# Kernel optimization log

Hardware: AMD Instinct MI355X
Metric: run time of the kernel (lower is better)

Reference implementation:

```python
import jax, jax.numpy as jnp
import numpy as np

N, n, m, k = 100000, 32, 16, 32
MU = 100.0  # bubble kernel scale (init arg mu)


def setup_inputs() -> dict:
    key = jax.random.key(0)
    ks = jax.random.split(key, 7)
    x = jax.random.normal(ks[0], (N,), dtype=jnp.float32)
    # torch.nn.Linear(N, n): weight [n, N], bias [n]
    encoder_w = jax.random.normal(ks[1], (n, N), dtype=jnp.float32) / np.float32(np.sqrt(N))
    encoder_b = jnp.zeros((n,), dtype=jnp.float32)
    # decoder parameter [n, N]
    decoder = jax.random.normal(ks[2], (n, N), dtype=jnp.float32) / np.float32(np.sqrt(n))
    # torch.nn.Linear(n, n*m): weight [n*m, n], bias [n*m]
    bw_w = jax.random.normal(ks[3], (n * m, n), dtype=jnp.float32) / np.float32(np.sqrt(n))
    bw_b = jnp.zeros((n * m,), dtype=jnp.float32)
    neighbour_distance = jax.random.uniform(ks[4], (N, k), dtype=jnp.float32)
    neighbour_id = jax.random.randint(ks[5], (N, k), 0, N)
    clustering_labels = jax.random.randint(ks[6], (N,), 0, m)
    return {
        "x": x,
        "encoder_w": encoder_w,
        "encoder_b": encoder_b,
        "decoder": decoder,
        "bw_w": bw_w,
        "bw_b": bw_b,
        "neighbour_distance": neighbour_distance,
        "neighbour_id": neighbour_id,
        "clustering_labels": clustering_labels,
    }


def reference(x, encoder_w, encoder_b, decoder, bw_w, bw_b,
              neighbour_distance, neighbour_id, clustering_labels):
    # encode: [N] -> [n]
    encoded = x @ encoder_w.T + encoder_b
    # per-basis, per-cluster bandwidths: sigmoid(Linear)/60 -> [n, m] -> expand to [n, N]
    bandwidths = jax.nn.sigmoid(encoded @ bw_w.T + bw_b) / 60.0
    w = bandwidths.reshape(n, m)[:, clustering_labels]  # [n, N]
    # bubble window: relu(1 - d^2 / (w*mu)^2) -> [n, N, k]
    window = jax.nn.relu(1.0 - neighbour_distance[None, :, :] ** 2
                         / (w[:, :, None] * MU) ** 2)
    # normalization over axis 1 (the N axis), faithful to the source's dim=1
    window = window / jnp.sum(window, axis=1, keepdims=True)
    # gather decoder rows at neighbours, weight, reduce over k: [n, N]
    convolved_basis = jnp.sum(decoder[:, neighbour_id] * window, axis=-1)
    # [n] @ [n, N] -> [N]
    return encoded @ convolved_basis
```

## Files before the change

### kernel.cpp

```cpp
#include <hip/hip_runtime.h>
#include <hip/hip_fp16.h>

#define N_PTS 100000
#define MU_F  100.0f
#define BUCKET 8192

typedef unsigned int uint;
typedef _Float16 h2 __attribute__((ext_vector_type(2)));
typedef float f2 __attribute__((ext_vector_type(2)));

#define E_SCALE 16384.0f
#define E_SCALE_INV (1.0f / 16384.0f)

static __device__ inline h2 h2pack(float a, float b) {
    return __builtin_bit_cast(h2, __builtin_amdgcn_cvt_pkrtz(a, b));
}
static __device__ inline float fdot2f(h2 a, h2 b, float c) {
    return __builtin_amdgcn_fdot2(a, b, c, false);
}
static __device__ inline h2 h2fma(h2 a, h2 b, h2 c) {
#if __has_builtin(__builtin_elementwise_fma)
    return __builtin_elementwise_fma(a, b, c);
#else
    return a * b + c;
#endif
}
static __device__ inline h2 h2max(h2 a, h2 b) {
#if __has_builtin(__builtin_elementwise_max)
    return __builtin_elementwise_max(a, b);
#else
    h2 r;
    r.x = a.x > b.x ? a.x : b.x;
    r.y = a.y > b.y ? a.y : b.y;
    return r;
#endif
}

#define ENC_BLKS 800
#define TR_BLKS  1563
#define SC_BLKS  196

__global__ __launch_bounds__(256) void k_prep(const float* __restrict__ x,
                                              const float* __restrict__ encW,
                                              const float* __restrict__ encB,
                                              const float* __restrict__ dec,
                                              const int* __restrict__ labels,
                                              float* __restrict__ enc,
                                              __half* __restrict__ decT,
                                              int* __restrict__ gcur,
                                              int* __restrict__ perm) {
    int b = blockIdx.x;
    if (b < ENC_BLKS) {
        int row = b & 31;
        int chunk = b >> 5;
        const int CH = 4000;
        int base = chunk * CH;
        const float4* W4 = reinterpret_cast<const float4*>(encW + (size_t)row * N_PTS + base);
        const float4* x4 = reinterpret_cast<const float4*>(x + base);
        const int nv = CH / 4;
        float acc = 0.f;
        for (int idx = threadIdx.x; idx < nv; idx += 256) {
            float4 w = W4[idx];
            float4 xv = x4[idx];
            acc += w.x * xv.x + w.y * xv.y + w.z * xv.z + w.w * xv.w;
        }
        #pragma unroll
        for (int off = 32; off > 0; off >>= 1) acc += __shfl_down(acc, off);
        __shared__ float sred[4];
        int wid = threadIdx.x >> 6;
        if ((threadIdx.x & 63) == 0) sred[wid] = acc;
        __syncthreads();
        if (threadIdx.x == 0) {
            float s = sred[0] + sred[1] + sred[2] + sred[3];
            if (chunk == 0) s += encB[row];
            atomicAdd(enc + row, s);
        }
    } else if (b < ENC_BLKS + TR_BLKS) {
        __shared__ float tile[32][65];
        int j0 = (b - ENC_BLKS) * 64;
        int col = threadIdx.x & 63;
        int r0 = threadIdx.x >> 6;
        #pragma unroll
        for (int it = 0; it < 8; ++it) {
            int row = it * 4 + r0;
            int j = j0 + col;
            float v = (j < N_PTS) ? dec[(size_t)row * N_PTS + j] : 0.f;
            tile[row][col] = v;
        }
        __syncthreads();
        #pragma unroll
        for (int it = 0; it < 4; ++it) {
            int idx = it * 256 + threadIdx.x;
            int j = idx >> 4;
            int p = idx & 15;
            int jj = j0 + j;
            if (jj < N_PTS) {
                __half2 h = __halves2half2(__float2half(tile[2 * p][j]),
                                           __float2half(tile[2 * p + 1][j]));
                *reinterpret_cast<__half2*>(decT + (size_t)jj * 32 + 2 * p) = h;
            }
        }
    } else {
        __shared__ int lh[16], lbase[16], lcur[16];
        const int CHUNK = 512;
        int start = (b - ENC_BLKS - TR_BLKS) * CHUNK;
        int end = min(start + CHUNK, N_PTS);
        if (threadIdx.x < 16) { lh[threadIdx.x] = 0; lcur[threadIdx.x] = 0; }
        __syncthreads();
        for (int j = start + threadIdx.x; j < end; j += 256)
            atomicAdd(&lh[labels[j]], 1);
        __syncthreads();
        if (threadIdx.x < 16)
            lbase[threadIdx.x] = threadIdx.x * BUCKET +
                                 atomicAdd(&gcur[threadIdx.x], lh[threadIdx.x]);
        __syncthreads();
        for (int j = start + threadIdx.x; j < end; j += 256) {
            int c = labels[j];
            int lpos = atomicAdd(&lcur[c], 1);
            perm[lbase[c] + lpos] = j;
        }
    }
}

__device__ inline void build_invC(const float* __restrict__ encL,
                                  const float* __restrict__ bw_w,
                                  const float* __restrict__ bw_b,
                                  float* __restrict__ invCL, int c) {
    if (threadIdx.x < 32) {
        int r = threadIdx.x * 16 + c;
        float z = bw_b[r];
        const float* wr = bw_w + r * 32;
        #pragma unroll
        for (int p = 0; p < 32; ++p) z = fmaf(encL[p], wr[p], z);
        float s = 1.f / (1.f + __expf(-z));
        float wmu = s * (MU_F / 60.0f);
        invCL[threadIdx.x] = 1.f / (wmu * wmu);
    }
}

__global__ __launch_bounds__(256, 4) void k_S_sorted(const float* __restrict__ enc_g,
                                                     const float* __restrict__ bw_w,
                                                     const float* __restrict__ bw_b,
                                                     const float* __restrict__ nd,
                                                     const int* __restrict__ perm,
                                                     const int* __restrict__ gcur,
                                                     float* __restrict__ S) {
    __shared__ float encL[32], invCL[32];
    __shared__ float Sloc[1024];
    int b = blockIdx.x;
    int c = b & 15;
    int ch = b >> 4;
    if (threadIdx.x < 32) encL[threadIdx.x] = enc_g[threadIdx.x];
    for (int t = threadIdx.x; t < 1024; t += 256) Sloc[t] = 0.f;
    __syncthreads();
    build_invC(encL, bw_w, bw_b, invCL, c);
    __syncthreads();

    f2 inv2[16];
    #pragma unroll
    for (int t = 0; t < 16; ++t) { inv2[t].x = invCL[2 * t]; inv2[t].y = invCL[2 * t + 1]; }

    int bs = c * BUCKET;
    int cnt = gcur[c];
    int lane = threadIdx.x & 63;
    int kk = lane & 31;
    int jh = lane >> 5;
    int gw = ch * 4 + (threadIdx.x >> 6);
    const int nw = 64 * 4;
    int npairs = (cnt + 1) >> 1;

    f2 acc2[16];
    #pragma unroll
    for (int t = 0; t < 16; ++t) { acc2[t].x = 0.f; acc2[t].y = 0.f; }

    if (gw < npairs) {
        auto ld = [&](int pc, float& d, bool& v) {
            bool ok = pc < npairs;
            v = ok && (2 * pc + jh) < cnt;
            int p = v ? (bs + 2 * pc + jh) : bs;
            int j = __builtin_nontemporal_load(&perm[p]);
            d = __builtin_nontemporal_load(&nd[(size_t)j * 32 + kk]);
        };
        int pp = gw;
        float dA, dB; bool vA, vB;
        ld(pp, dA, vA);
        ld(pp + nw, dB, vB);
        while (pp < npairs) {
            float dC; bool vC;
            ld(pp + 2 * nw, dC, vC);
            float d2 = vA ? dA * dA : 1e30f;
            f2 md2; md2.x = -d2; md2.y = -d2;
            f2 onev; onev.x = 1.f; onev.y = 1.f;
            #pragma unroll
            for (int t = 0; t < 16; ++t) {
                f2 w = md2 * inv2[t] + onev;
                w.x = fmaxf(w.x, 0.f);
                w.y = fmaxf(w.y, 0.f);
                acc2[t] += w;
            }
            dA = dB; vA = vB; dB = dC; vB = vC;
            pp += nw;
        }
    }
    #pragma unroll
    for (int t = 0; t < 16; ++t) {
        acc2[t].x += __shfl_xor(acc2[t].x, 32);
        acc2[t].y += __shfl_xor(acc2[t].y, 32);
    }
    if (jh == 0) {
        #pragma unroll
        for (int t = 0; t < 16; ++t) {
            atomicAdd(&Sloc[(2 * t) * 32 + kk], acc2[t].x);
            atomicAdd(&Sloc[(2 * t + 1) * 32 + kk], acc2[t].y);
        }
    }
    __syncthreads();
    for (int t = threadIdx.x; t < 1024; t += 256) {
        float v = Sloc[t];
        if (v != 0.f) atomicAdd(&S[t], v);
    }
}

__global__ __launch_bounds__(256, 8) void k_main(const float* __restrict__ enc_g,
                                                 const float* __restrict__ bw_w,
                                                 const float* __restrict__ bw_b,
                                                 const float* __restrict__ S_g,
                                                 const float* __restrict__ nd,
                                                 const int* __restrict__ nid,
                                                 const int* __restrict__ perm,
                                                 const int* __restrict__ gcur,
                                                 const __half* __restrict__ decT,
                                                 float* __restrict__ out) {
    __shared__ float encL[32], invCL[32];
    __shared__ float ELf[1024];
    int c = blockIdx.x & 15;
    int ch = blockIdx.x >> 4;
    if (threadIdx.x < 32) encL[threadIdx.x] = enc_g[threadIdx.x];
    __syncthreads();
    build_invC(encL, bw_w, bw_b, invCL, c);
    for (int t = threadIdx.x; t < 1024; t += 256)
        ELf[t] = encL[t >> 5] / S_g[t] * E_SCALE;
    __syncthreads();

    int lane = threadIdx.x & 63;
    int R = lane >> 2;
    int q = lane & 3;

    h2 invh[4], EhA[4], EhB[4];
    #pragma unroll
    for (int t = 0; t < 4; ++t) {
        int i0 = q * 8 + 2 * t;
        invh[t] = h2pack(fminf(invCL[i0], 6.0e4f), fminf(invCL[i0 + 1], 6.0e4f));
        EhA[t] = h2pack(ELf[i0 * 32 + R], ELf[(i0 + 1) * 32 + R]);
        EhB[t] = h2pack(ELf[i0 * 32 + R + 16], ELf[(i0 + 1) * 32 + R + 16]);
    }
    const h2 zero2 = h2pack(0.f, 0.f);
    const h2 one2 = h2pack(1.f, 1.f);

    int bs = c * BUCKET;
    int cnt = gcur[c];
    int wv = ch * 4 + (threadIdx.x >> 6);
    const int nw = 128 * 4;
    int npairs = (cnt + 1) >> 1;
    const uint4* decQ = reinterpret_cast<const uint4*>(decT);
    if (wv >= npairs) return;

    auto load_pair = [&](int pp, int& j0, int& j1, bool& v1) {
        bool ok = pp < npairs;
        int p0 = ok ? (bs + 2 * pp) : bs;
        v1 = ok && ((2 * pp + 1) < cnt);
        j0 = perm[p0];
        j1 = perm[v1 ? p0 + 1 : p0];
    };
    auto load_ids = [&](int j0, int j1, int* id, float* dd) {
        #pragma unroll
        for (int s = 0; s < 4; ++s) {
            int jj = (s >> 1) ? j1 : j0;
            size_t idx = (size_t)jj * 32 + (s & 1) * 16 + R;
            id[s] = __builtin_nontemporal_load(&nid[idx]);
            dd[s] = __builtin_nontemporal_load(&nd[idx]);
        }
    };

    int pp = wv;
    int j0a, j1a, j0b, j1b; bool v1a, v1b;
    int ida[4]; float dda[4];
    load_pair(pp, j0a, j1a, v1a);
    load_ids(j0a, j1a, ida, dda);
    load_pair(pp + nw, j0b, j1b, v1b);

    while (pp < npairs) {
        uint4 r0 = decQ[(size_t)ida[0] * 4 + q];
        uint4 r1 = decQ[(size_t)ida[1] * 4 + q];
        uint4 r2 = decQ[(size_t)ida[2] * 4 + q];
        uint4 r3 = decQ[(size_t)ida[3] * 4 + q];
        int idb[4]; float ddb[4];
        load_ids(j0b, j1b, idb, ddb);
        int j0c, j1c; bool v1c;
        load_pair(pp + 2 * nw, j0c, j1c, v1c);

        float d20 = dda[0] * dda[0];
        float d21 = dda[1] * dda[1];
        float d22 = dda[2] * dda[2];
        float d23 = dda[3] * dda[3];
        h2 md0 = h2pack(-d20, -d20);
        h2 md1 = h2pack(-d21, -d21);
        h2 md2 = h2pack(-d22, -d22);
        h2 md3 = h2pack(-d23, -d23);

        float a0 = 0.f, a1 = 0.f, a2 = 0.f, a3 = 0.f;
        #pragma unroll
        for (int t = 0; t < 4; ++t) {
            uint dw0 = (t == 0) ? r0.x : (t == 1) ? r0.y : (t == 2) ? r0.z : r0.w;
            uint dw1 = (t == 0) ? r1.x : (t == 1) ? r1.y : (t == 2) ? r1.z : r1.w;
            uint dw2 = (t == 0) ? r2.x : (t == 1) ? r2.y : (t == 2) ? r2.z : r2.w;
            uint dw3 = (t == 0) ? r3.x : (t == 1) ? r3.y : (t == 2) ? r3.z : r3.w;
            {
                h2 w = h2max(h2fma(md0, invh[t], one2), zero2);
                a0 = fdot2f(w * EhA[t], __builtin_bit_cast(h2, dw0), a0);
            }
            {
                h2 w = h2max(h2fma(md1, invh[t], one2), zero2);
                a1 = fdot2f(w * EhB[t], __builtin_bit_cast(h2, dw1), a1);
            }
            {
                h2 w = h2max(h2fma(md2, invh[t], one2), zero2);
                a2 = fdot2f(w * EhA[t], __builtin_bit_cast(h2, dw2), a2);
            }
            {
                h2 w = h2max(h2fma(md3, invh[t], one2), zero2);
                a3 = fdot2f(w * EhB[t], __builtin_bit_cast(h2, dw3), a3);
            }
        }
        float u = a0 + a1;
        float v = a2 + a3;
        #pragma unroll
        for (int off = 32; off > 0; off >>= 1) {
            u += __shfl_xor(u, off);
            v += __shfl_xor(v, off);
        }
        if (lane == 0) __builtin_nontemporal_store(u * E_SCALE_INV, &out[j0a]);
        if (lane == 32 && v1a) __builtin_nontemporal_store(v * E_SCALE_INV, &out[j1a]);

        j0a = j0b; j1a = j1b; v1a = v1b;
        j0b = j0c; j1b = j1c; v1b = v1c;
        #pragma unroll
        for (int s = 0; s < 4; ++s) { ida[s] = idb[s]; dda[s] = ddb[s]; }
        pp += nw;
    }
}

extern "C" void kernel_launch(void* const* d_in, const int* in_sizes, int n_in,
                              void* d_out, int out_size, void* d_ws, size_t ws_size,
                              hipStream_t stream) {
    const float* x     = (const float*)d_in[0];
    const float* enc_w = (const float*)d_in[1];
    const float* enc_b = (const float*)d_in[2];
    const float* dec   = (const float*)d_in[3];
    const float* bw_w  = (const float*)d_in[4];
    const float* bw_b  = (const float*)d_in[5];
    const float* nd    = (const float*)d_in[6];
    const int*   nid   = (const int*)d_in[7];
    const int*   labels= (const int*)d_in[8];
    float* out = (float*)d_out;

    char* ws = (char*)d_ws;
    float* enc    = (float*)(ws + 0);
    float* S      = (float*)(ws + 128);
    int* gcur     = (int*)(ws + 4224);
    int* perm     = (int*)(ws + 8192);
    __half* decT  = (__half*)(ws + 532480);

    (void)hipMemsetAsync(d_ws, 0, 4288, stream);
    k_prep<<<dim3(ENC_BLKS + TR_BLKS + SC_BLKS), dim3(256), 0, stream>>>(
        x, enc_w, enc_b, dec, labels, enc, decT, gcur, perm);
    k_S_sorted<<<dim3(1024), dim3(256), 0, stream>>>(enc, bw_w, bw_b, nd, perm,
                                                     gcur, S);
    k_main<<<dim3(2048), dim3(256), 0, stream>>>(enc, bw_w, bw_b, S, nd, nid,
                                                 perm, gcur, decT, out);
}
```

Baseline: 182.0 us.

## Split S accumulation into per-chunk partials, retune grids and load pipelining

Replaces global atomics into a single 1024-entry S with atomics into per-chunk slices (128 slices), followed by a new small reduction kernel. Doubles the S-kernel grid and raises its occupancy bound, and restructures its prefetch so the perm index is loaded two steps ahead and the distance one step ahead. It also shrinks the main kernel grid and occupancy hint and switches output stores from nontemporal to normal. These target atomic contention and latency hiding, but add a large memset of the partial buffer and an extra kernel launch.

```diff
diff --git a/kernel.cpp b/kernel.cpp
--- a/kernel.cpp
+++ b/kernel.cpp
@@ -138,13 +138,13 @@
     }
 }
 
-__global__ __launch_bounds__(256, 4) void k_S_sorted(const float* __restrict__ enc_g,
+__global__ __launch_bounds__(256, 8) void k_S_sorted(const float* __restrict__ enc_g,
                                                      const float* __restrict__ bw_w,
                                                      const float* __restrict__ bw_b,
                                                      const float* __restrict__ nd,
                                                      const int* __restrict__ perm,
                                                      const int* __restrict__ gcur,
-                                                     float* __restrict__ S) {
+                                                     float* __restrict__ S_part) {
     __shared__ float encL[32], invCL[32];
     __shared__ float Sloc[1024];
     int b = blockIdx.x;
@@ -166,7 +166,7 @@
     int kk = lane & 31;
     int jh = lane >> 5;
     int gw = ch * 4 + (threadIdx.x >> 6);
-    const int nw = 64 * 4;
+    const int nw = 128 * 4;
     int npairs = (cnt + 1) >> 1;
 
     f2 acc2[16];
@@ -174,20 +174,19 @@
     for (int t = 0; t < 16; ++t) { acc2[t].x = 0.f; acc2[t].y = 0.f; }
 
     if (gw < npairs) {
-        auto ld = [&](int pc, float& d, bool& v) {
-            bool ok = pc < npairs;
-            v = ok && (2 * pc + jh) < cnt;
+        auto ldj = [&](int pc) -> int {
+            bool v = (pc < npairs) && ((2 * pc + jh) < cnt);
             int p = v ? (bs + 2 * pc + jh) : bs;
-            int j = __builtin_nontemporal_load(&perm[p]);
-            d = __builtin_nontemporal_load(&nd[(size_t)j * 32 + kk]);
+            return __builtin_nontemporal_load(&perm[p]);
         };
         int pp = gw;
-        float dA, dB; bool vA, vB;
-        ld(pp, dA, vA);
-        ld(pp + nw, dB, vB);
+        int jA = ldj(pp);
+        float dA = __builtin_nontemporal_load(&nd[(size_t)jA * 32 + kk]);
+        int jB = ldj(pp + nw);
         while (pp < npairs) {
-            float dC; bool vC;
-            ld(pp + 2 * nw, dC, vC);
+            float dB = __builtin_nontemporal_load(&nd[(size_t)jB * 32 + kk]);
+            int jC = ldj(pp + 2 * nw);
+            bool vA = (2 * pp + jh) < cnt;
             float d2 = vA ? dA * dA : 1e30f;
             f2 md2; md2.x = -d2; md2.y = -d2;
             f2 onev; onev.x = 1.f; onev.y = 1.f;
@@ -198,7 +197,7 @@
                 w.y = fmaxf(w.y, 0.f);
                 acc2[t] += w;
             }
-            dA = dB; vA = vB; dB = dC; vB = vC;
+            dA = dB; jB = jC;
             pp += nw;
         }
     }
@@ -215,13 +214,24 @@
         }
     }
     __syncthreads();
+    float* slice = S_part + (size_t)ch * 1024;
     for (int t = threadIdx.x; t < 1024; t += 256) {
         float v = Sloc[t];
-        if (v != 0.f) atomicAdd(&S[t], v);
-    }
-}
-
-__global__ __launch_bounds__(256, 8) void k_main(const float* __restrict__ enc_g,
+        if (v != 0.f) atomicAdd(&slice[t], v);
+    }
+}
+
+__global__ __launch_bounds__(256) void k_S_red(const float* __restrict__ S_part,
+                                               float* __restrict__ S) {
+    int t = blockIdx.x * 256 + threadIdx.x;
+    float s = 0.f;
+    #pragma unroll
+    for (int u = 0; u < 128; ++u)
+        s += S_part[(size_t)u * 1024 + t];
+    S[t] = s;
+}
+
+__global__ __launch_bounds__(256, 6) void k_main(const float* __restrict__ enc_g,
                                                  const float* __restrict__ bw_w,
                                                  const float* __restrict__ bw_b,
                                                  const float* __restrict__ S_g,
@@ -260,7 +270,7 @@
     int bs = c * BUCKET;
     int cnt = gcur[c];
     int wv = ch * 4 + (threadIdx.x >> 6);
-    const int nw = 128 * 4;
+    const int nw = 96 * 4;
     int npairs = (cnt + 1) >> 1;
     const uint4* decQ = reinterpret_cast<const uint4*>(decT);
     if (wv >= npairs) return;
@@ -339,8 +349,8 @@
             u += __shfl_xor(u, off);
             v += __shfl_xor(v, off);
         }
-        if (lane == 0) __builtin_nontemporal_store(u * E_SCALE_INV, &out[j0a]);
-        if (lane == 32 && v1a) __builtin_nontemporal_store(v * E_SCALE_INV, &out[j1a]);
+        if (lane == 0) out[j0a] = u * E_SCALE_INV;
+        if (lane == 32 && v1a) out[j1a] = v * E_SCALE_INV;
 
         j0a = j0b; j1a = j1b; v1a = v1b;
         j0b = j0c; j1b = j1c; v1b = v1c;
@@ -366,16 +376,18 @@
 
     char* ws = (char*)d_ws;
     float* enc    = (float*)(ws + 0);
-    float* S      = (float*)(ws + 128);
-    int* gcur     = (int*)(ws + 4224);
-    int* perm     = (int*)(ws + 8192);
-    __half* decT  = (__half*)(ws + 532480);
-
-    (void)hipMemsetAsync(d_ws, 0, 4288, stream);
+    int* gcur     = (int*)(ws + 128);
+    float* S_part = (float*)(ws + 4096);
+    float* S      = (float*)(ws + 528384);
+    int* perm     = (int*)(ws + 532480);
+    __half* decT  = (__half*)(ws + 1056768);
+
+    (void)hipMemsetAsync(d_ws, 0, 528384, stream);
     k_prep<<<dim3(ENC_BLKS + TR_BLKS + SC_BLKS), dim3(256), 0, stream>>>(
         x, enc_w, enc_b, dec, labels, enc, decT, gcur, perm);
-    k_S_sorted<<<dim3(1024), dim3(256), 0, stream>>>(enc, bw_w, bw_b, nd, perm,
-                                                     gcur, S);
-    k_main<<<dim3(2048), dim3(256), 0, stream>>>(enc, bw_w, bw_b, S, nd, nid,
+    k_S_sorted<<<dim3(2048), dim3(256), 0, stream>>>(enc, bw_w, bw_b, nd, perm,
+                                                     gcur, S_part);
+    k_S_red<<<dim3(4), dim3(256), 0, stream>>>(S_part, S);
+    k_main<<<dim3(1536), dim3(256), 0, stream>>>(enc, bw_w, bw_b, S, nd, nid,
                                                  perm, gcur, decT, out);
 }
```

After: 258.1 us. +41.8%, slower.
